# Performance work log

Measured on AMD Instinct MI355X. Metric: run time of the kernel, lower is better.

Reference implementation:

```python
import jax, jax.numpy as jnp
import numpy as np

B, N, DIM = 4, 1024, 1024
HEADS, DH = 16, 64
INNER = HEADS * DH          # 1024
PROJ_H = max(16, DH // 8)   # 16
TOP_K = 256
TEMP = 1.0
SCALE = DH ** -0.5
LN_EPS = 1e-5


def setup_inputs() -> dict:
    key = jax.random.key(0)
    ks = jax.random.split(key, 9)
    s = 0.02
    return {
        "x": jax.random.normal(ks[0], (B, N, DIM), dtype=jnp.float32),
        "w_qkv": jax.random.normal(ks[1], (3 * INNER, DIM), dtype=jnp.float32) * s,
        "w_out": jax.random.normal(ks[2], (DIM, INNER), dtype=jnp.float32) * s,
        "b_out": jnp.zeros((DIM,), dtype=jnp.float32),
        "ln_g": jnp.ones((DH,), dtype=jnp.float32),
        "ln_b": jnp.zeros((DH,), dtype=jnp.float32),
        "w1": jax.random.normal(ks[3], (PROJ_H, DH), dtype=jnp.float32) * s,
        "b1": jnp.zeros((PROJ_H,), dtype=jnp.float32),
        "w2": jax.random.normal(ks[4], (1, PROJ_H), dtype=jnp.float32) * s,
        "b2": jnp.zeros((1,), dtype=jnp.float32),
    }


def _soma_gate(token_feat, ln_g, ln_b, w1, b1, w2, b2):
    # token_feat: [B, N, DH] -> gate [B, N] in (0,1)
    mu = token_feat.mean(axis=-1, keepdims=True)
    var = token_feat.var(axis=-1, keepdims=True)
    H = (token_feat - mu) * jax.lax.rsqrt(var + LN_EPS) * ln_g + ln_b
    h = jax.nn.gelu(H @ w1.T + b1, approximate=False)
    scores = (h @ w2.T + b2)[..., 0]                       # [B, N]
    scores = scores / (TEMP + 1e-12)
    # top-k soft mask: non-topk positions set to -1e9 before sigmoid
    topk_vals, topk_idx = jax.lax.top_k(scores, TOP_K)
    b_idx = jnp.arange(scores.shape[0])[:, None]
    scores = jnp.full_like(scores, -1e9).at[b_idx, topk_idx].set(topk_vals)
    return jax.nn.sigmoid(scores)


def reference(x, w_qkv, w_out, b_out, ln_g, ln_b, w1, b1, w2, b2):
    Bx, Nx, _ = x.shape
    qkv = x @ w_qkv.T                                      # [B, N, 3*INNER]
    q, k, v = jnp.split(qkv, 3, axis=-1)
    to_heads = lambda t: t.reshape(Bx, Nx, HEADS, DH).transpose(0, 2, 1, 3)
    q, k, v = to_heads(q), to_heads(k), to_heads(v)        # [B, H, N, DH]

    dots = jnp.einsum('bhid,bhjd->bhij', q, k) * SCALE     # [B, H, N, N]

    q_mean = q.mean(axis=1)                                # [B, N, DH]
    gate = _soma_gate(q_mean, ln_g, ln_b, w1, b1, w2, b2)  # [B, N]
    dots = dots * (gate[:, None, :, None] * gate[:, None, None, :])

    attn = jax.nn.softmax(dots, axis=-1)
    out = jnp.einsum('bhij,bhjd->bhid', attn, v)           # [B, H, N, DH]
    out = out.transpose(0, 2, 1, 3).reshape(Bx, Nx, INNER)
    return out @ w_out.T + b_out
```

## Files before the change

### kernel.cpp

```cpp
#include <hip/hip_runtime.h>
#include <hip/hip_bf16.h>
#include <stdint.h>

typedef __bf16 bf16;
typedef __bf16 bf16x8 __attribute__((ext_vector_type(8)));
typedef float floatx4 __attribute__((ext_vector_type(4)));

typedef const __attribute__((address_space(1))) uint32_t glb_u32;
typedef __attribute__((address_space(3))) uint32_t lds_u32;

__device__ __forceinline__ void cp16(void* lds, const void* gp) {
    __builtin_amdgcn_global_load_lds((glb_u32*)gp, (lds_u32*)lds, 16, 0, 0);
}

#define MFMA16(a, b, c) __builtin_amdgcn_mfma_f32_16x16x32_bf16((a), (b), (c), 0, 0, 0)
#define SCALE_ 0.125f

__global__ __launch_bounds__(256) void k_cvt_prep(
    const float* __restrict__ x, const float* __restrict__ wq,
    const float* __restrict__ wo, bf16* __restrict__ xb,
    bf16* __restrict__ wqb, bf16* __restrict__ wob,
    float* __restrict__ wqmT) {
    if (blockIdx.x < 4096) {
        size_t i8 = ((size_t)blockIdx.x * 256 + threadIdx.x) * 8;
        const float* src; bf16* dst; size_t off;
        if (i8 < 4194304)      { src = x;  dst = xb;  off = i8; }
        else if (i8 < 7340032) { src = wq; dst = wqb; off = i8 - 4194304; }
        else                   { src = wo; dst = wob; off = i8 - 7340032; }
        float4 a = *(const float4*)(src + off);
        float4 b = *(const float4*)(src + off + 4);
        union { bf16 h[8]; uint4 u; } tmp;
        tmp.h[0] = (bf16)a.x; tmp.h[1] = (bf16)a.y; tmp.h[2] = (bf16)a.z; tmp.h[3] = (bf16)a.w;
        tmp.h[4] = (bf16)b.x; tmp.h[5] = (bf16)b.y; tmp.h[6] = (bf16)b.z; tmp.h[7] = (bf16)b.w;
        *(uint4*)(dst + off) = tmp.u;
    } else {
        int t = (blockIdx.x - 4096) * 256 + threadIdx.x;
        int k = t & 1023, d = t >> 10;
        float s = 0.f;
        #pragma unroll
        for (int h = 0; h < 16; ++h) s += wq[(size_t)(h * 64 + d) * 1024 + k];
        wqmT[k * 64 + d] = s * (1.f / 16.f);
    }
}

__global__ __launch_bounds__(256) void k_score(
    const float* __restrict__ xf, const float* __restrict__ wqmT,
    const float* __restrict__ lng, const float* __restrict__ lnb,
    const float* __restrict__ w1f, const float* __restrict__ b1f,
    const float* __restrict__ w2f, const float* __restrict__ b2f,
    float* __restrict__ scores) {
    const int w = threadIdx.x >> 6, lane = threadIdx.x & 63;
    const int r0 = blockIdx.x * 8;
    const int k0 = w * 256;
    __shared__ float part[4][8][64];
    __shared__ float qm_s[8][64];
    __shared__ float Hs[4][64];
    __shared__ float hh[4][16];

    float acc[8];
    #pragma unroll
    for (int i = 0; i < 8; ++i) acc[i] = 0.f;

    for (int k = k0; k < k0 + 256; k += 4) {
        float w0 = wqmT[(k + 0) * 64 + lane];
        float w1 = wqmT[(k + 1) * 64 + lane];
        float w2 = wqmT[(k + 2) * 64 + lane];
        float w3 = wqmT[(k + 3) * 64 + lane];
        #pragma unroll
        for (int i = 0; i < 8; ++i) {
            float4 xv = *(const float4*)(xf + (size_t)(r0 + i) * 1024 + k);
            acc[i] += xv.x * w0; acc[i] += xv.y * w1;
            acc[i] += xv.z * w2; acc[i] += xv.w * w3;
        }
    }
    #pragma unroll
    for (int i = 0; i < 8; ++i) part[w][i][lane] = acc[i];
    __syncthreads();
    for (int e = threadIdx.x; e < 512; e += 256) {
        int r = e >> 6, d = e & 63;
        qm_s[r][d] = part[0][r][d] + part[1][r][d] + part[2][r][d] + part[3][r][d];
    }
    __syncthreads();

    for (int i = 0; i < 2; ++i) {
        const int r = w * 2 + i;
        float qm = qm_s[r][lane];
        float s = qm;
        #pragma unroll
        for (int off = 32; off > 0; off >>= 1) s += __shfl_xor(s, off);
        float mu = s * (1.f / 64.f);
        float dx = qm - mu;
        float v2 = dx * dx;
        #pragma unroll
        for (int off = 32; off > 0; off >>= 1) v2 += __shfl_xor(v2, off);
        float var = v2 * (1.f / 64.f);
        float H = dx * (1.0f / sqrtf(var + 1e-5f)) * lng[lane] + lnb[lane];
        Hs[w][lane] = H;
        if (lane < 16) {
            float a = b1f[lane];
            #pragma unroll
            for (int d = 0; d < 64; ++d) a += Hs[w][d] * w1f[lane * 64 + d];
            hh[w][lane] = 0.5f * a * (1.0f + erff(a * 0.70710678118654752f));
        }
        if (lane == 0) {
            float sc = b2f[0];
            #pragma unroll
            for (int p = 0; p < 16; ++p) sc += hh[w][p] * w2f[p];
            scores[r0 + r] = sc;
        }
    }
}

__global__ __launch_bounds__(256) void k_topk(const float* __restrict__ scores,
                                              float* __restrict__ gate,
                                              int* __restrict__ idx,
                                              float* __restrict__ gsel) {
    const int w = threadIdx.x >> 6, lane = threadIdx.x & 63;
    const float* sc = scores + w * 1024;
    float s[16];
    uint32_t key[16];
    #pragma unroll
    for (int i = 0; i < 16; ++i) {
        s[i] = sc[lane * 16 + i];
        uint32_t u = __float_as_uint(s[i]);
        key[i] = (u >> 31) ? ~u : (u | 0x80000000u);
    }
    uint32_t prefix = 0;
    for (int bit = 31; bit >= 0; --bit) {
        uint32_t cand = prefix | (1u << bit);
        int c = 0;
        #pragma unroll
        for (int i = 0; i < 16; ++i) c += (key[i] >= cand);
        #pragma unroll
        for (int off = 1; off < 64; off <<= 1) c += __shfl_xor(c, off);
        if (c >= 256) prefix = cand;
    }
    int cg = 0, eq = 0;
    #pragma unroll
    for (int i = 0; i < 16; ++i) { cg += (key[i] > prefix); eq += (key[i] == prefix); }
    #pragma unroll
    for (int off = 1; off < 64; off <<= 1) cg += __shfl_xor(cg, off);
    const int quota = 256 - cg;
    int xs = eq;
    #pragma unroll
    for (int off = 1; off < 64; off <<= 1) {
        int y = __shfl_up(xs, off);
        if (lane >= off) xs += y;
    }
    int run = xs - eq;
    bool selv[16];
    int cnt = 0;
    #pragma unroll
    for (int i = 0; i < 16; ++i) {
        bool sel = key[i] > prefix;
        if (key[i] == prefix) { sel = (run < quota); run++; }
        selv[i] = sel;
        cnt += sel ? 1 : 0;
        gate[w * 1024 + lane * 16 + i] = sel ? 1.0f / (1.0f + expf(-s[i])) : 0.0f;
    }
    int xc = cnt;
    #pragma unroll
    for (int off = 1; off < 64; off <<= 1) {
        int y = __shfl_up(xc, off);
        if (lane >= off) xc += y;
    }
    int pos = xc - cnt;
    #pragma unroll
    for (int i = 0; i < 16; ++i) {
        if (selv[i]) {
            idx[w * 256 + pos]  = lane * 16 + i;
            gsel[w * 256 + pos] = 1.0f / (1.0f + expf(-s[i]));
            pos++;
        }
    }
}

__global__ __launch_bounds__(256) void k_qkv_sel(
    const bf16* __restrict__ xb, const bf16* __restrict__ wqb,
    const int* __restrict__ idx, bf16* __restrict__ qsel,
    bf16* __restrict__ ksel, bf16* __restrict__ vbuf) {
    __shared__ bf16 As[128 * 32];
    __shared__ bf16 Bs[128 * 32];
    const int t = threadIdx.x;
    const int lane = t & 63;
    const int w = t >> 6;
    const int srow = t >> 2;
    const int scol = (t & 3) * 8;
    const int wm = (w & 1) * 64;
    const int wn = (w >> 1) * 64;
    const int fr = lane & 15;
    const int kc = (lane >> 4) * 8;

    const int bid = blockIdx.x;
    const bool isV = bid < 256;
    int n0, m0;
    size_t abase1, abase2;
    const bf16* Bsrc;
    if (isV) {
        n0 = (bid & 7) * 128;
        m0 = (bid >> 3) * 128;
        Bsrc = wqb + (size_t)(2048 + n0) * 1024;
        abase1 = (size_t)(m0 + srow) * 1024;
        abase2 = (size_t)(m0 + srow + 64) * 1024;
    } else {
        int q = bid - 256;
        n0 = (q & 15) * 128;
        m0 = (q >> 4) * 128;
        Bsrc = wqb + (size_t)n0 * 1024;
        const int mg1 = m0 + srow, mg2 = mg1 + 64;
        const int tok1 = idx[(mg1 >> 8) * 256 + (mg1 & 255)];
        const int tok2 = idx[(mg2 >> 8) * 256 + (mg2 & 255)];
        abase1 = ((size_t)(mg1 >> 8) * 1024 + tok1) * 1024;
        abase2 = ((size_t)(mg2 >> 8) * 1024 + tok2) * 1024;
    }

    floatx4 zero4 = {0.f, 0.f, 0.f, 0.f};
    floatx4 acc[4][4];
    #pragma unroll
    for (int i = 0; i < 4; ++i)
        #pragma unroll
        for (int j = 0; j < 4; ++j) acc[i][j] = zero4;

    for (int k0 = 0; k0 < 1024; k0 += 32) {
        __syncthreads();
        cp16(As + t * 8,        xb + abase1 + k0 + scol);
        cp16(As + t * 8 + 2048, xb + abase2 + k0 + scol);
        cp16(Bs + t * 8,        Bsrc + (size_t)srow * 1024 + k0 + scol);
        cp16(Bs + t * 8 + 2048, Bsrc + (size_t)(srow + 64) * 1024 + k0 + scol);
        __syncthreads();
        bf16x8 a[4], b[4];
        #pragma unroll
        for (int mi = 0; mi < 4; ++mi)
            a[mi] = *(const bf16x8*)&As[(wm + mi * 16 + fr) * 32 + kc];
        #pragma unroll
        for (int ni = 0; ni < 4; ++ni)
            b[ni] = *(const bf16x8*)&Bs[(wn + ni * 16 + fr) * 32 + kc];
        #pragma unroll
        for (int mi = 0; mi < 4; ++mi)
            #pragma unroll
            for (int ni = 0; ni < 4; ++ni)
                acc[mi][ni] = MFMA16(a[mi], b[ni], acc[mi][ni]);
    }

    const int rowb = (lane >> 4) * 4;
    #pragma unroll
    for (int ni = 0; ni < 4; ++ni) {
        const int n_base = n0 + wn + ni * 16;
        if (isV) {
            const int h = n_base >> 6;
            const int dd = (n_base & 63) + fr;
            #pragma unroll
            for (int mi = 0; mi < 4; ++mi)
                #pragma unroll
                for (int r = 0; r < 4; ++r) {
                    const int mg = m0 + wm + mi * 16 + rowb + r;
                    const int bb = mg >> 10, nq = mg & 1023;
                    vbuf[(((size_t)(bb * 16 + h)) * 1024 + nq) * 64 + dd] =
                        (bf16)acc[mi][ni][r];
                }
        } else {
            const int region = n_base >> 10;
            const int nn = n_base & 1023;
            const int h = nn >> 6;
            const int dd = (nn & 63) + fr;
            #pragma unroll
            for (int mi = 0; mi < 4; ++mi)
                #pragma unroll
                for (int r = 0; r < 4; ++r) {
                    const int mg = m0 + wm + mi * 16 + rowb + r;
                    const bf16 v = (bf16)acc[mi][ni][r];
                    if (region == 0) {
                        qsel[(size_t)mg * 1024 + h * 64 + dd] = v;
                    } else {
                        const int b = mg >> 8, s = mg & 255;
                        ksel[(((size_t)(b * 16 + h)) * 256 + s) * 64 + dd] = v;
                    }
                }
        }
    }
}

__global__ __launch_bounds__(256) void k_vgather(
    const bf16* __restrict__ vbuf, const int* __restrict__ idx,
    bf16* __restrict__ VselT, float* __restrict__ SumVuns,
    bf16* __restrict__ qsel) {
    const int bh = blockIdx.x, b = bh >> 4, h = bh & 15;
    const int t = threadIdx.x, w = t >> 6, lane = t & 63;
    const bf16* vb = vbuf + (size_t)bh * 65536;
    bf16* Vo = VselT + (size_t)bh * 16384;

    __shared__ bf16 Vt[64][72];
    __shared__ float redAll[4][64];
    __shared__ float redSel[4][64];

    float sAll = 0.f;
    for (int j = w * 256; j < w * 256 + 256; ++j)
        sAll += (float)vb[(size_t)j * 64 + lane];
    redAll[w][lane] = sAll;

    const int d = t & 63, sg = t >> 6;
    const int s_loc = t >> 2, part = t & 3;
    float sSel = 0.f;

    for (int c = 0; c < 4; ++c) {
        __syncthreads();
        int j = idx[b * 256 + c * 64 + s_loc];
        const uint4* vsrc = (const uint4*)(vb + (size_t)j * 64 + part * 16);
        uint4 v0 = vsrc[0], v1 = vsrc[1];
        *(uint4*)&Vt[s_loc][part * 16]     = v0;
        *(uint4*)&Vt[s_loc][part * 16 + 8] = v1;
        __syncthreads();
        union { bf16 h_[16]; uint4 u[2]; } tmp;
        #pragma unroll
        for (int u = 0; u < 16; ++u) {
            bf16 v = Vt[sg * 16 + u][d];
            tmp.h_[u] = v;
            sSel += (float)v;
        }
        uint4* vdst = (uint4*)(Vo + (size_t)d * 256 + c * 64 + sg * 16);
        vdst[0] = tmp.u[0]; vdst[1] = tmp.u[1];
    }
    redSel[sg][d] = sSel;
    __syncthreads();
    if (t < 64) {
        float sa = redAll[0][t] + redAll[1][t] + redAll[2][t] + redAll[3][t];
        float ss = redSel[0][t] + redSel[1][t] + redSel[2][t] + redSel[3][t];
        SumVuns[bh * 64 + t] = sa - ss;
        qsel[(size_t)(1024 + b) * 1024 + h * 64 + t] = (bf16)(sa * (1.f / 1024.f));
    }
}

__global__ __launch_bounds__(256) void k_attn(
    bf16* __restrict__ qsel, const bf16* __restrict__ Ksel,
    const bf16* __restrict__ VselT, const float* __restrict__ gsel,
    const float* __restrict__ SumVuns) {
    const int bh = blockIdx.x;
    const int qt = blockIdx.y;
    const int b = bh >> 4, h = bh & 15;
    const int t = threadIdx.x, w = t >> 6, lane = t & 63;
    const int m0 = qt * 64;
    const bf16* kb = Ksel + (size_t)bh * 16384;
    const bf16* vb = VselT + (size_t)bh * 16384;

    __shared__ bf16 Qs[64 * 72];
    __shared__ bf16 Ks[64 * 72];
    __shared__ bf16 Vs[64 * 72];
    __shared__ bf16 Ps[4][16 * 72];

    #pragma unroll
    for (int c = 0; c < 2; ++c) {
        int idx2 = t + 256 * c, row = idx2 >> 3, c8 = (idx2 & 7) * 8;
        *(uint4*)&Qs[row * 72 + c8] =
            *(const uint4*)&qsel[(size_t)(b * 256 + m0 + row) * 1024 + h * 64 + c8];
    }
    const int fr = lane & 15;
    const int kq = lane >> 4;
    const int rowb = kq * 4;
    __syncthreads();
    bf16x8 aq[2];
    aq[0] = *(const bf16x8*)&Qs[(w * 16 + fr) * 72 + kq * 8];
    aq[1] = *(const bf16x8*)&Qs[(w * 16 + fr) * 72 + 32 + kq * 8];

    float gq[4];
    #pragma unroll
    for (int r = 0; r < 4; ++r)
        gq[r] = gsel[b * 256 + m0 + w * 16 + rowb + r] * SCALE_;

    float mrow[4] = {0.f, 0.f, 0.f, 0.f};
    float lrow[4] = {0.f, 0.f, 0.f, 0.f};
    floatx4 zero4 = {0.f, 0.f, 0.f, 0.f};
    floatx4 Of[4] = {zero4, zero4, zero4, zero4};

    for (int jt = 0; jt < 4; ++jt) {
        const int j0 = jt * 64;
        __syncthreads();
        #pragma unroll
        for (int c = 0; c < 2; ++c) {
            int idx2 = t + 256 * c, row = idx2 >> 3, c8 = (idx2 & 7) * 8;
            *(uint4*)&Ks[row * 72 + c8] = *(const uint4*)&kb[(size_t)(j0 + row) * 64 + c8];
            *(uint4*)&Vs[row * 72 + c8] = *(const uint4*)&vb[(size_t)row * 256 + j0 + c8];
        }
        __syncthreads();

        floatx4 S[4] = {zero4, zero4, zero4, zero4};
        #pragma unroll
        for (int ks = 0; ks < 2; ++ks) {
            #pragma unroll
            for (int ni = 0; ni < 4; ++ni) {
                bf16x8 bfr = *(const bf16x8*)&Ks[(ni * 16 + fr) * 72 + ks * 32 + kq * 8];
                S[ni] = MFMA16(aq[ks], bfr, S[ni]);
            }
        }
        float gk[4];
        #pragma unroll
        for (int ni = 0; ni < 4; ++ni) gk[ni] = gsel[b * 256 + j0 + ni * 16 + fr];

        float p[4][4], rmax[4] = {0.f, 0.f, 0.f, 0.f};
        #pragma unroll
        for (int ni = 0; ni < 4; ++ni)
            #pragma unroll
            for (int r = 0; r < 4; ++r) {
                float sv = S[ni][r] * (gq[r] * gk[ni]);
                p[ni][r] = sv;
                rmax[r] = fmaxf(rmax[r], sv);
            }
        #pragma unroll
        for (int r = 0; r < 4; ++r) {
            #pragma unroll
            for (int off = 1; off < 16; off <<= 1)
                rmax[r] = fmaxf(rmax[r], __shfl_xor(rmax[r], off));
        }
        float alpha[4], rsum[4] = {0.f, 0.f, 0.f, 0.f};
        #pragma unroll
        for (int r = 0; r < 4; ++r) {
            float mn = fmaxf(mrow[r], rmax[r]);
            alpha[r] = __expf(mrow[r] - mn);
            mrow[r] = mn;
        }
        #pragma unroll
        for (int ni = 0; ni < 4; ++ni)
            #pragma unroll
            for (int r = 0; r < 4; ++r) {
                float pv = __expf(p[ni][r] - mrow[r]);
                p[ni][r] = pv;
                rsum[r] += pv;
            }
        #pragma unroll
        for (int r = 0; r < 4; ++r) {
            #pragma unroll
            for (int off = 1; off < 16; off <<= 1) rsum[r] += __shfl_xor(rsum[r], off);
            lrow[r] = lrow[r] * alpha[r] + rsum[r];
        }
        #pragma unroll
        for (int nd = 0; nd < 4; ++nd)
            #pragma unroll
            for (int r = 0; r < 4; ++r) Of[nd][r] *= alpha[r];

        #pragma unroll
        for (int ni = 0; ni < 4; ++ni)
            #pragma unroll
            for (int r = 0; r < 4; ++r)
                Ps[w][(rowb + r) * 72 + ni * 16 + fr] = (bf16)p[ni][r];

        #pragma unroll
        for (int ks = 0; ks < 2; ++ks) {
            bf16x8 ap = *(const bf16x8*)&Ps[w][fr * 72 + ks * 32 + kq * 8];
            #pragma unroll
            for (int nd = 0; nd < 4; ++nd) {
                bf16x8 bv = *(const bf16x8*)&Vs[(nd * 16 + fr) * 72 + ks * 32 + kq * 8];
                Of[nd] = MFMA16(ap, bv, Of[nd]);
            }
        }
    }

    #pragma unroll
    for (int nd = 0; nd < 4; ++nd)
        #pragma unroll
        for (int r = 0; r < 4; ++r) {
            float em = __expf(-mrow[r]);
            float num = Of[nd][r] + em * SumVuns[bh * 64 + nd * 16 + fr];
            float den = lrow[r] + 768.0f * em;
            qsel[(size_t)(b * 256 + m0 + w * 16 + rowb + r) * 1024 +
                 h * 64 + nd * 16 + fr] = (bf16)(num / den);
        }
}

__global__ __launch_bounds__(256) void k_out_sel(
    const bf16* __restrict__ A, const bf16* __restrict__ wob,
    const float* __restrict__ b_out, const int* __restrict__ idx,
    float* __restrict__ ubase, float* __restrict__ out) {
    __shared__ bf16 As[128 * 32];
    __shared__ bf16 Bs[128 * 32];
    const int t = threadIdx.x;
    const int lane = t & 63;
    const int w = t >> 6;
    const int n0 = blockIdx.x * 128;
    const int m0 = blockIdx.y * 128;
    const bf16* Bsrc = wob + (size_t)n0 * 1024;

    const int srow = t >> 2;
    const int scol = (t & 3) * 8;
    const int wm = (w & 1) * 64;
    const int wn = (w >> 1) * 64;
    const int fr = lane & 15;
    const int kc = (lane >> 4) * 8;

    floatx4 zero4 = {0.f, 0.f, 0.f, 0.f};
    floatx4 acc[4][4];
    #pragma unroll
    for (int i = 0; i < 4; ++i)
        #pragma unroll
        for (int j = 0; j < 4; ++j) acc[i][j] = zero4;

    for (int k0 = 0; k0 < 1024; k0 += 32) {
        __syncthreads();
        cp16(As + t * 8,        A + (size_t)(m0 + srow) * 1024 + k0 + scol);
        cp16(As + t * 8 + 2048, A + (size_t)(m0 + srow + 64) * 1024 + k0 + scol);
        cp16(Bs + t * 8,        Bsrc + (size_t)srow * 1024 + k0 + scol);
        cp16(Bs + t * 8 + 2048, Bsrc + (size_t)(srow + 64) * 1024 + k0 + scol);
        __syncthreads();
        bf16x8 a[4], b[4];
        #pragma unroll
        for (int mi = 0; mi < 4; ++mi)
            a[mi] = *(const bf16x8*)&As[(wm + mi * 16 + fr) * 32 + kc];
        #pragma unroll
        for (int ni = 0; ni < 4; ++ni)
            b[ni] = *(const bf16x8*)&Bs[(wn + ni * 16 + fr) * 32 + kc];
        #pragma unroll
        for (int mi = 0; mi < 4; ++mi)
            #pragma unroll
            for (int ni = 0; ni < 4; ++ni)
                acc[mi][ni] = MFMA16(a[mi], b[ni], acc[mi][ni]);
    }

    const int rowb = (lane >> 4) * 4;
    #pragma unroll
    for (int ni = 0; ni < 4; ++ni) {
        const int ng = n0 + wn + ni * 16 + fr;
        const float bias = b_out[ng];
        #pragma unroll
        for (int mi = 0; mi < 4; ++mi)
            #pragma unroll
            for (int r = 0; r < 4; ++r) {
                const int mg = m0 + wm + mi * 16 + rowb + r;
                const float val = acc[mi][ni][r] + bias;
                if (mg < 1024) {
                    const int b = mg >> 8, s = mg & 255;
                    const int tok = idx[b * 256 + s];
                    out[((size_t)b * 1024 + tok) * 1024 + ng] = val;
                } else if (mg < 1028) {
                    ubase[(size_t)(mg - 1024) * 1024 + ng] = val;
                }
            }
    }
}

__global__ __launch_bounds__(256) void k_fill(
    const float* __restrict__ gate, const float* __restrict__ ubase,
    float* __restrict__ out) {
    const int tokg = blockIdx.x;
    if (gate[tokg] > 0.f) return;
    const int b = tokg >> 10;
    const int c = threadIdx.x * 4;
    *(float4*)(out + (size_t)tokg * 1024 + c) = *(const float4*)(ubase + b * 1024 + c);
}

extern "C" void kernel_launch(void* const* d_in, const int* in_sizes, int n_in,
                              void* d_out, int out_size, void* d_ws, size_t ws_size,
                              hipStream_t stream) {
    const float* x     = (const float*)d_in[0];
    const float* w_qkv = (const float*)d_in[1];
    const float* w_out = (const float*)d_in[2];
    const float* b_out = (const float*)d_in[3];
    const float* ln_g  = (const float*)d_in[4];
    const float* ln_b  = (const float*)d_in[5];
    const float* w1    = (const float*)d_in[6];
    const float* b1    = (const float*)d_in[7];
    const float* w2    = (const float*)d_in[8];
    const float* b2    = (const float*)d_in[9];
    float* out = (float*)d_out;

    char* ws = (char*)d_ws;
    bf16*  qsel  = (bf16*)(ws);
    bf16*  ksel  = (bf16*)(ws + 4194304);
    bf16*  VselT = (bf16*)(ws + 6291456);
    bf16*  vbuf  = (bf16*)(ws + 8388608);
    bf16*  xb    = (bf16*)(ws + 16777216);
    bf16*  wqb   = (bf16*)(ws + 25165824);
    bf16*  wob   = (bf16*)(ws + 31457280);
    float* wqmT    = (float*)(ws + 33554432);
    int*   idx     = (int*)(ws + 33816576);
    float* gsel    = (float*)(ws + 33820672);
    float* scores  = (float*)(ws + 33824768);
    float* gate    = (float*)(ws + 33841152);
    float* SumVuns = (float*)(ws + 33857536);
    float* ubase   = (float*)(ws + 33873920);

    k_cvt_prep<<<4352, 256, 0, stream>>>(x, w_qkv, w_out, xb, wqb, wob, wqmT);
    k_score<<<512, 256, 0, stream>>>(x, wqmT, ln_g, ln_b, w1, b1, w2, b2, scores);
    k_topk<<<1, 256, 0, stream>>>(scores, gate, idx, gsel);
    k_qkv_sel<<<384, 256, 0, stream>>>(xb, wqb, idx, qsel, ksel, vbuf);
    k_vgather<<<64, 256, 0, stream>>>(vbuf, idx, VselT, SumVuns, qsel);
    k_attn<<<dim3(64, 4), 256, 0, stream>>>(qsel, ksel, VselT, gsel, SumVuns);
    k_out_sel<<<dim3(8, 9), 256, 0, stream>>>(qsel, wob, b_out, idx, ubase, out);
    k_fill<<<4096, 256, 0, stream>>>(gate, ubase, out);
}
```

Before: 237.2 us.

## Compute gate scores with split-bf16 MFMA GEMM instead of scalar FP32 loop

Replaces the FP32 scalar-FMA score projection (x times head-averaged Wq) with an MFMA GEMM that uses a hi/lo bf16 split of both x and the averaged weight, which keeps roughly FP32 accuracy for the top-k selection. The prep kernel now also writes the bf16 low residual of x and the hi/lo split of the averaged weights. The LayerNorm/MLP tail moves to a separate kernel. This adds an extra 8MB write and a kernel launch, and the GEMM runs on only 32 blocks, so it may underuse the GPU.

```diff
diff --git a/kernel.cpp b/kernel.cpp
--- a/kernel.cpp
+++ b/kernel.cpp
@@ -19,95 +19,142 @@
 __global__ __launch_bounds__(256) void k_cvt_prep(
     const float* __restrict__ x, const float* __restrict__ wq,
     const float* __restrict__ wo, bf16* __restrict__ xb,
-    bf16* __restrict__ wqb, bf16* __restrict__ wob,
-    float* __restrict__ wqmT) {
+    bf16* __restrict__ xl, bf16* __restrict__ wqb, bf16* __restrict__ wob,
+    bf16* __restrict__ whl) {
     if (blockIdx.x < 4096) {
         size_t i8 = ((size_t)blockIdx.x * 256 + threadIdx.x) * 8;
-        const float* src; bf16* dst; size_t off;
-        if (i8 < 4194304)      { src = x;  dst = xb;  off = i8; }
+        const float* src; bf16* dst; size_t off; bool isx = false;
+        if (i8 < 4194304)      { src = x;  dst = xb;  off = i8; isx = true; }
         else if (i8 < 7340032) { src = wq; dst = wqb; off = i8 - 4194304; }
         else                   { src = wo; dst = wob; off = i8 - 7340032; }
         float4 a = *(const float4*)(src + off);
         float4 b = *(const float4*)(src + off + 4);
-        union { bf16 h[8]; uint4 u; } tmp;
-        tmp.h[0] = (bf16)a.x; tmp.h[1] = (bf16)a.y; tmp.h[2] = (bf16)a.z; tmp.h[3] = (bf16)a.w;
-        tmp.h[4] = (bf16)b.x; tmp.h[5] = (bf16)b.y; tmp.h[6] = (bf16)b.z; tmp.h[7] = (bf16)b.w;
-        *(uint4*)(dst + off) = tmp.u;
+        union { bf16 h[8]; uint4 u; } hi, lo;
+        hi.h[0] = (bf16)a.x; hi.h[1] = (bf16)a.y; hi.h[2] = (bf16)a.z; hi.h[3] = (bf16)a.w;
+        hi.h[4] = (bf16)b.x; hi.h[5] = (bf16)b.y; hi.h[6] = (bf16)b.z; hi.h[7] = (bf16)b.w;
+        *(uint4*)(dst + off) = hi.u;
+        if (isx) {
+            lo.h[0] = (bf16)(a.x - (float)hi.h[0]);
+            lo.h[1] = (bf16)(a.y - (float)hi.h[1]);
+            lo.h[2] = (bf16)(a.z - (float)hi.h[2]);
+            lo.h[3] = (bf16)(a.w - (float)hi.h[3]);
+            lo.h[4] = (bf16)(b.x - (float)hi.h[4]);
+            lo.h[5] = (bf16)(b.y - (float)hi.h[5]);
+            lo.h[6] = (bf16)(b.z - (float)hi.h[6]);
+            lo.h[7] = (bf16)(b.w - (float)hi.h[7]);
+            *(uint4*)(xl + off) = lo.u;
+        }
     } else {
         int t = (blockIdx.x - 4096) * 256 + threadIdx.x;
         int k = t & 1023, d = t >> 10;
         float s = 0.f;
         #pragma unroll
         for (int h = 0; h < 16; ++h) s += wq[(size_t)(h * 64 + d) * 1024 + k];
-        wqmT[k * 64 + d] = s * (1.f / 16.f);
-    }
-}
-
-__global__ __launch_bounds__(256) void k_score(
-    const float* __restrict__ xf, const float* __restrict__ wqmT,
-    const float* __restrict__ lng, const float* __restrict__ lnb,
-    const float* __restrict__ w1f, const float* __restrict__ b1f,
-    const float* __restrict__ w2f, const float* __restrict__ b2f,
-    float* __restrict__ scores) {
+        s *= (1.f / 16.f);
+        bf16 hi = (bf16)s;
+        whl[(size_t)d * 1024 + k] = hi;
+        whl[(size_t)(64 + d) * 1024 + k] = (bf16)(s - (float)hi);
+    }
+}
+
+__global__ __launch_bounds__(256) void k_score_gemm(
+    const bf16* __restrict__ xh, const bf16* __restrict__ xl,
+    const bf16* __restrict__ whl, float* __restrict__ qmbuf) {
+    __shared__ bf16 Ah[128 * 32];
+    __shared__ bf16 Al[128 * 32];
+    __shared__ bf16 Bs[128 * 32];
+    const int t = threadIdx.x;
+    const int lane = t & 63;
+    const int w = t >> 6;
+    const int m0 = blockIdx.x * 128;
+    const int srow = t >> 2;
+    const int scol = (t & 3) * 8;
+    const int fr = lane & 15;
+    const int kc = (lane >> 4) * 8;
+    const int wm0 = w * 32;
+
+    floatx4 zero4 = {0.f, 0.f, 0.f, 0.f};
+    floatx4 acc[2][4];
+    #pragma unroll
+    for (int i = 0; i < 2; ++i)
+        #pragma unroll
+        for (int j = 0; j < 4; ++j) acc[i][j] = zero4;
+
+    for (int k0 = 0; k0 < 1024; k0 += 32) {
+        __syncthreads();
+        cp16(Ah + t * 8,        xh + (size_t)(m0 + srow) * 1024 + k0 + scol);
+        cp16(Ah + t * 8 + 2048, xh + (size_t)(m0 + srow + 64) * 1024 + k0 + scol);
+        cp16(Al + t * 8,        xl + (size_t)(m0 + srow) * 1024 + k0 + scol);
+        cp16(Al + t * 8 + 2048, xl + (size_t)(m0 + srow + 64) * 1024 + k0 + scol);
+        cp16(Bs + t * 8,        whl + (size_t)srow * 1024 + k0 + scol);
+        cp16(Bs + t * 8 + 2048, whl + (size_t)(srow + 64) * 1024 + k0 + scol);
+        __syncthreads();
+        bf16x8 ah[2], al[2], bh[4], bl[4];
+        #pragma unroll
+        for (int mi = 0; mi < 2; ++mi) {
+            ah[mi] = *(const bf16x8*)&Ah[(wm0 + mi * 16 + fr) * 32 + kc];
+            al[mi] = *(const bf16x8*)&Al[(wm0 + mi * 16 + fr) * 32 + kc];
+        }
+        #pragma unroll
+        for (int ni = 0; ni < 4; ++ni) {
+            bh[ni] = *(const bf16x8*)&Bs[(ni * 16 + fr) * 32 + kc];
+            bl[ni] = *(const bf16x8*)&Bs[(64 + ni * 16 + fr) * 32 + kc];
+        }
+        #pragma unroll
+        for (int mi = 0; mi < 2; ++mi)
+            #pragma unroll
+            for (int ni = 0; ni < 4; ++ni) {
+                acc[mi][ni] = MFMA16(ah[mi], bh[ni], acc[mi][ni]);
+                acc[mi][ni] = MFMA16(ah[mi], bl[ni], acc[mi][ni]);
+                acc[mi][ni] = MFMA16(al[mi], bh[ni], acc[mi][ni]);
+            }
+    }
+
+    const int rowb = (lane >> 4) * 4;
+    #pragma unroll
+    for (int mi = 0; mi < 2; ++mi)
+        #pragma unroll
+        for (int ni = 0; ni < 4; ++ni)
+            #pragma unroll
+            for (int r = 0; r < 4; ++r) {
+                const int row = m0 + wm0 + mi * 16 + rowb + r;
+                qmbuf[(size_t)row * 64 + ni * 16 + fr] = acc[mi][ni][r];
+            }
+}
+
+__global__ __launch_bounds__(256) void k_score_tail(
+    const float* __restrict__ qmbuf, const float* __restrict__ lng,
+    const float* __restrict__ lnb, const float* __restrict__ w1f,
+    const float* __restrict__ b1f, const float* __restrict__ w2f,
+    const float* __restrict__ b2f, float* __restrict__ scores) {
     const int w = threadIdx.x >> 6, lane = threadIdx.x & 63;
-    const int r0 = blockIdx.x * 8;
-    const int k0 = w * 256;
-    __shared__ float part[4][8][64];
-    __shared__ float qm_s[8][64];
+    const int r = blockIdx.x * 4 + w;
     __shared__ float Hs[4][64];
     __shared__ float hh[4][16];
 
-    float acc[8];
-    #pragma unroll
-    for (int i = 0; i < 8; ++i) acc[i] = 0.f;
-
-    for (int k = k0; k < k0 + 256; k += 4) {
-        float w0 = wqmT[(k + 0) * 64 + lane];
-        float w1 = wqmT[(k + 1) * 64 + lane];
-        float w2 = wqmT[(k + 2) * 64 + lane];
-        float w3 = wqmT[(k + 3) * 64 + lane];
-        #pragma unroll
-        for (int i = 0; i < 8; ++i) {
-            float4 xv = *(const float4*)(xf + (size_t)(r0 + i) * 1024 + k);
-            acc[i] += xv.x * w0; acc[i] += xv.y * w1;
-            acc[i] += xv.z * w2; acc[i] += xv.w * w3;
-        }
-    }
-    #pragma unroll
-    for (int i = 0; i < 8; ++i) part[w][i][lane] = acc[i];
-    __syncthreads();
-    for (int e = threadIdx.x; e < 512; e += 256) {
-        int r = e >> 6, d = e & 63;
-        qm_s[r][d] = part[0][r][d] + part[1][r][d] + part[2][r][d] + part[3][r][d];
-    }
-    __syncthreads();
-
-    for (int i = 0; i < 2; ++i) {
-        const int r = w * 2 + i;
-        float qm = qm_s[r][lane];
-        float s = qm;
-        #pragma unroll
-        for (int off = 32; off > 0; off >>= 1) s += __shfl_xor(s, off);
-        float mu = s * (1.f / 64.f);
-        float dx = qm - mu;
-        float v2 = dx * dx;
-        #pragma unroll
-        for (int off = 32; off > 0; off >>= 1) v2 += __shfl_xor(v2, off);
-        float var = v2 * (1.f / 64.f);
-        float H = dx * (1.0f / sqrtf(var + 1e-5f)) * lng[lane] + lnb[lane];
-        Hs[w][lane] = H;
-        if (lane < 16) {
-            float a = b1f[lane];
-            #pragma unroll
-            for (int d = 0; d < 64; ++d) a += Hs[w][d] * w1f[lane * 64 + d];
-            hh[w][lane] = 0.5f * a * (1.0f + erff(a * 0.70710678118654752f));
-        }
-        if (lane == 0) {
-            float sc = b2f[0];
-            #pragma unroll
-            for (int p = 0; p < 16; ++p) sc += hh[w][p] * w2f[p];
-            scores[r0 + r] = sc;
-        }
+    float qm = qmbuf[(size_t)r * 64 + lane];
+    float s = qm;
+    #pragma unroll
+    for (int off = 32; off > 0; off >>= 1) s += __shfl_xor(s, off);
+    float mu = s * (1.f / 64.f);
+    float dx = qm - mu;
+    float v2 = dx * dx;
+    #pragma unroll
+    for (int off = 32; off > 0; off >>= 1) v2 += __shfl_xor(v2, off);
+    float var = v2 * (1.f / 64.f);
+    float H = dx * (1.0f / sqrtf(var + 1e-5f)) * lng[lane] + lnb[lane];
+    Hs[w][lane] = H;
+    if (lane < 16) {
+        float a = b1f[lane];
+        #pragma unroll
+        for (int d = 0; d < 64; ++d) a += Hs[w][d] * w1f[lane * 64 + d];
+        hh[w][lane] = 0.5f * a * (1.0f + erff(a * 0.70710678118654752f));
+    }
+    if (lane == 0) {
+        float sc = b2f[0];
+        #pragma unroll
+        for (int p = 0; p < 16; ++p) sc += hh[w][p] * w2f[p];
+        scores[r] = sc;
     }
 }
 
@@ -568,16 +615,19 @@
     bf16*  xb    = (bf16*)(ws + 16777216);
     bf16*  wqb   = (bf16*)(ws + 25165824);
     bf16*  wob   = (bf16*)(ws + 31457280);
-    float* wqmT    = (float*)(ws + 33554432);
-    int*   idx     = (int*)(ws + 33816576);
-    float* gsel    = (float*)(ws + 33820672);
-    float* scores  = (float*)(ws + 33824768);
-    float* gate    = (float*)(ws + 33841152);
-    float* SumVuns = (float*)(ws + 33857536);
-    float* ubase   = (float*)(ws + 33873920);
-
-    k_cvt_prep<<<4352, 256, 0, stream>>>(x, w_qkv, w_out, xb, wqb, wob, wqmT);
-    k_score<<<512, 256, 0, stream>>>(x, wqmT, ln_g, ln_b, w1, b1, w2, b2, scores);
+    int*   idx     = (int*)(ws + 33554432);
+    float* gsel    = (float*)(ws + 33558528);
+    float* scores  = (float*)(ws + 33562624);
+    float* gate    = (float*)(ws + 33579008);
+    float* SumVuns = (float*)(ws + 33595392);
+    float* ubase   = (float*)(ws + 33611776);
+    bf16*  whl     = (bf16*)(ws + 33685504);
+    float* qmbuf   = (float*)(ws + 34603008);
+    bf16*  xlbuf   = (bf16*)(ws + 35651584);
+
+    k_cvt_prep<<<4352, 256, 0, stream>>>(x, w_qkv, w_out, xb, xlbuf, wqb, wob, whl);
+    k_score_gemm<<<32, 256, 0, stream>>>(xb, xlbuf, whl, qmbuf);
+    k_score_tail<<<1024, 256, 0, stream>>>(qmbuf, ln_g, ln_b, w1, b1, w2, b2, scores);
     k_topk<<<1, 256, 0, stream>>>(scores, gate, idx, gsel);
     k_qkv_sel<<<384, 256, 0, stream>>>(xb, wqb, idx, qsel, ksel, vbuf);
     k_vgather<<<64, 256, 0, stream>>>(vbuf, idx, VselT, SumVuns, qsel);
```

Result: faster. 228.7 us, median of 2 (-3.6%).
